# Optimization experiments

Hardware: AMD Instinct MI355X
Metric: run time of the kernel (lower is better)

Reference implementation:

```python
import jax, jax.numpy as jnp
import numpy as np

N_NODES = 50000
N_EDGES = 800000
N_GRAPHS = 512
IN_DIM = 128
HID = 64


def setup_inputs() -> dict:
    key = jax.random.key(0)
    ks = jax.random.split(key, 12)
    x = jax.random.normal(ks[0], (N_NODES, IN_DIM), dtype=jnp.float32)
    edge_index = jax.random.randint(ks[1], (2, N_EDGES), 0, N_NODES, dtype=jnp.int64)
    batch = jnp.sort(jax.random.randint(ks[2], (N_NODES,), 0, N_GRAPHS, dtype=jnp.int64))

    def lin(k, fan_in, fan_out):
        # torch Linear default init: U(-1/sqrt(fan_in), 1/sqrt(fan_in)); stored as [in, out]
        bound = 1.0 / np.sqrt(fan_in)
        return jax.random.uniform(k, (fan_in, fan_out), minval=-bound, maxval=bound, dtype=jnp.float32)

    W1_1 = lin(ks[3], IN_DIM, HID)
    W2_1 = lin(ks[4], IN_DIM, HID)
    W1_2 = lin(ks[5], HID, HID)
    W2_2 = lin(ks[6], HID, HID)
    W1_3 = lin(ks[7], HID, HID)
    W2_3 = lin(ks[8], HID, HID)
    cW1 = lin(ks[9], HID, HID)
    cb1 = jnp.zeros((HID,), dtype=jnp.float32)
    cW2 = lin(ks[10], HID, 1)
    cb2 = jnp.zeros((1,), dtype=jnp.float32)
    return {"x": x, "edge_index": edge_index, "batch": batch,
            "W1_1": W1_1, "W2_1": W2_1, "W1_2": W1_2, "W2_2": W2_2,
            "W1_3": W1_3, "W2_3": W2_3, "cW1": cW1, "cb1": cb1,
            "cW2": cW2, "cb2": cb2}


def _gnn_layer(x, src, dst, W1, W2):
    # f(v) = relu( x[v] @ W1 + sum_{u in N(v)} x[u] @ W2 )
    self_part = x @ W1                      # [N, out]
    msg = x[src] @ W2                       # gather + matmul: [E, out]
    neigh = jax.ops.segment_sum(msg, dst, num_segments=N_NODES)  # scatter-add
    return jax.nn.relu(self_part + neigh)


def reference(x, edge_index, batch, W1_1, W2_1, W1_2, W2_2, W1_3, W2_3, cW1, cb1, cW2, cb2):
    src, dst = edge_index[0], edge_index[1]  # PyG source_to_target flow
    h = _gnn_layer(x, src, dst, W1_1, W2_1)
    h = _gnn_layer(h, src, dst, W1_2, W2_2)
    h = _gnn_layer(h, src, dst, W1_3, W2_3)
    # global_mean_pool over graph segments
    sums = jax.ops.segment_sum(h, batch, num_segments=N_GRAPHS)      # [G, HID]
    counts = jax.ops.segment_sum(jnp.ones((h.shape[0],), h.dtype), batch, num_segments=N_GRAPHS)
    pooled = sums / jnp.maximum(counts, 1.0)[:, None]
    # classifier MLP
    hcls = jax.nn.relu(pooled @ cW1 + cb1)
    return hcls @ cW2 + cb2                  # [G, 1]
```

## Files before the change

### kernel.cpp

```cpp
#include <hip/hip_runtime.h>


#define CAP 64

typedef __attribute__((ext_vector_type(8))) short short8;
typedef __attribute__((ext_vector_type(4))) float floatx4;

__device__ __forceinline__ unsigned short f2bf(float f) {
    union { float f; unsigned u; } v; v.f = f;
    unsigned r = v.u + 0x7FFF + ((v.u >> 16) & 1);
    return (unsigned short)(r >> 16);
}

__device__ __forceinline__ void bf8acc(float* t, uint4 w) {
    t[0] += __uint_as_float(w.x << 16);
    t[1] += __uint_as_float(w.x & 0xffff0000u);
    t[2] += __uint_as_float(w.y << 16);
    t[3] += __uint_as_float(w.y & 0xffff0000u);
    t[4] += __uint_as_float(w.z << 16);
    t[5] += __uint_as_float(w.z & 0xffff0000u);
    t[6] += __uint_as_float(w.w << 16);
    t[7] += __uint_as_float(w.w & 0xffff0000u);
}

__device__ __forceinline__ void gather_node(
    const unsigned short* __restrict__ M, const int* __restrict__ cnt,
    const unsigned short* __restrict__ csr, int node, int cg, float* acc8)
{
    int c = cnt[node]; if (c > CAP) c = CAP;
    const uint4* bv = (const uint4*)(csr + (size_t)node * CAP);
    float a[8], b[8];
#pragma unroll
    for (int j = 0; j < 8; ++j) { a[j] = 0.f; b[j] = 0.f; }
    const int full = c >> 3;
    const int rem  = c & 7;
    for (int grp = 0; grp < full; ++grp) {
        uint4 q = bv[grp];
        unsigned idx[8];
        idx[0] = q.x & 0xffff; idx[1] = q.x >> 16;
        idx[2] = q.y & 0xffff; idx[3] = q.y >> 16;
        idx[4] = q.z & 0xffff; idx[5] = q.z >> 16;
        idx[6] = q.w & 0xffff; idx[7] = q.w >> 16;
        uint4 w[8];
#pragma unroll
        for (int j = 0; j < 8; ++j)
            w[j] = *(const uint4*)&M[(size_t)idx[j] * 64 + cg * 8];
#pragma unroll
        for (int j = 0; j < 8; ++j)
            bf8acc((j & 1) ? b : a, w[j]);
    }
    if (rem) {
        uint4 q = bv[full];
        unsigned idx[8];
        idx[0] = q.x & 0xffff; idx[1] = q.x >> 16;
        idx[2] = q.y & 0xffff; idx[3] = q.y >> 16;
        idx[4] = q.z & 0xffff; idx[5] = q.z >> 16;
        idx[6] = q.w & 0xffff; idx[7] = q.w >> 16;
#pragma unroll
        for (int j = 0; j < 7; ++j) {
            if (j < rem) {
                uint4 w = *(const uint4*)&M[(size_t)idx[j] * 64 + cg * 8];
                bf8acc((j & 1) ? b : a, w);
            }
        }
    }
#pragma unroll
    for (int j = 0; j < 8; ++j) acc8[j] = a[j] + b[j];
}


__device__ __forceinline__ void mm1_body(
    const float* __restrict__ Xraw,
    const float* __restrict__ W1, const float* __restrict__ W2,
    float* __restrict__ S, unsigned short* __restrict__ M, int N, int blk)
{
    __shared__ __align__(16) unsigned short Xs[64][72];
    __shared__ __align__(16) unsigned short Ws[128][72];
    const int tid  = threadIdx.x;
    const int lane = tid & 63;
    const int wv   = tid >> 6;
    const int lrow = lane & 15;
    const int quad = lane >> 4;
    const int row0 = blk * 64;

    floatx4 acc[8];
#pragma unroll
    for (int i = 0; i < 8; ++i) acc[i] = (floatx4){0.f, 0.f, 0.f, 0.f};

    const int xr  = tid >> 2;
    const int xk  = (tid & 3) * 16;
    const int gxr = row0 + xr;

    for (int ko = 0; ko < 128; ko += 64) {
#pragma unroll
        for (int q = 0; q < 4; ++q) {
            float4 v = make_float4(0.f, 0.f, 0.f, 0.f);
            if (gxr < N) v = *(const float4*)&Xraw[(size_t)gxr * 128 + ko + xk + q * 4];
            ushort4 p;
            p.x = f2bf(v.x); p.y = f2bf(v.y); p.z = f2bf(v.z); p.w = f2bf(v.w);
            *(ushort4*)&Xs[xr][xk + q * 4] = p;
        }
#pragma unroll
        for (int i = 0; i < 2; ++i) {
            int s  = tid + i * 256;
            int k0 = (s & 15) * 4;
            int c0 = (s >> 4) * 4;
            float wr[4][4];
#pragma unroll
            for (int r = 0; r < 4; ++r) {
                int gk = ko + k0 + r;
                float4 t4 = (c0 < 64) ? *(const float4*)&W1[(size_t)gk * 64 + c0]
                                      : *(const float4*)&W2[(size_t)gk * 64 + (c0 - 64)];
                wr[r][0] = t4.x; wr[r][1] = t4.y; wr[r][2] = t4.z; wr[r][3] = t4.w;
            }
#pragma unroll
            for (int j = 0; j < 4; ++j) {
                ushort4 col;
                col.x = f2bf(wr[0][j]); col.y = f2bf(wr[1][j]);
                col.z = f2bf(wr[2][j]); col.w = f2bf(wr[3][j]);
                *(ushort4*)&Ws[c0 + j][k0] = col;
            }
        }
        __syncthreads();

#pragma unroll
        for (int kc = 0; kc < 2; ++kc) {
            int kofs = kc * 32 + quad * 8;
            short8 a = *(const short8*)&Xs[wv * 16 + lrow][kofs];
#pragma unroll
            for (int ct = 0; ct < 8; ++ct) {
                short8 b = *(const short8*)&Ws[ct * 16 + lrow][kofs];
                acc[ct] = __builtin_amdgcn_mfma_f32_16x16x32_bf16(a, b, acc[ct], 0, 0, 0);
            }
        }
        __syncthreads();
    }

    const int orow = row0 + wv * 16 + quad * 4;
#pragma unroll
    for (int ct = 0; ct < 4; ++ct) {
        int col = ct * 16 + lrow;
#pragma unroll
        for (int r = 0; r < 4; ++r) {
            int gr = orow + r;
            if (gr < N) S[(size_t)gr * 64 + col] = acc[ct][r];
        }
    }
#pragma unroll
    for (int ct = 4; ct < 8; ++ct) {
        int col = ct * 16 + lrow - 64;
#pragma unroll
        for (int r = 0; r < 4; ++r) {
            int gr = orow + r;
            if (gr < N) M[(size_t)gr * 64 + col] = f2bf(acc[ct][r]);
        }
    }
}

__device__ __forceinline__ void fill_body(
    const int* __restrict__ ei, int* __restrict__ cnt,
    unsigned short* __restrict__ csr, int E, int bid, int stride)
{
    int base = bid * 256 + threadIdx.x;
    int e[8], d[8], s[8], p[8];
    bool v[8];
#pragma unroll
    for (int j = 0; j < 8; ++j) {
        e[j] = base + j * stride;
        v[j] = e[j] < E;
        if (v[j]) {
            d[j] = ei[E + e[j]];
            s[j] = ei[e[j]];
        }
    }
#pragma unroll
    for (int j = 0; j < 8; ++j)
        if (v[j]) p[j] = atomicAdd(&cnt[d[j]], 1);
#pragma unroll
    for (int j = 0; j < 8; ++j)
        if (v[j] && p[j] < CAP) csr[(size_t)d[j] * CAP + p[j]] = (unsigned short)s[j];
}

__global__ __launch_bounds__(256) void mm1_fill_kernel(
    const float* __restrict__ Xraw,
    const float* __restrict__ W1, const float* __restrict__ W2,
    float* __restrict__ S, unsigned short* __restrict__ M, int N,
    const int* __restrict__ ei, int* __restrict__ cnt,
    unsigned short* __restrict__ csr, int E, int edgeBlocks)
{
    if ((int)blockIdx.x < edgeBlocks) {
        fill_body(ei, cnt, csr, E, blockIdx.x, edgeBlocks * 256);
    } else {
        mm1_body(Xraw, W1, W2, S, M, N, (int)blockIdx.x - edgeBlocks);
    }
}

__global__ __launch_bounds__(256) void mm_gather_kernel(
    const float* __restrict__ Sprev, const unsigned short* __restrict__ Mprev,
    const int* __restrict__ cnt, const unsigned short* __restrict__ csr,
    const float* __restrict__ W1, const float* __restrict__ W2,
    float* __restrict__ Sout, unsigned short* __restrict__ Mout, int N)
{
    __shared__ __align__(16) unsigned short Xs[64][72];
    __shared__ __align__(16) unsigned short Ws[128][72];
    const int tid  = threadIdx.x;
    const int lane = tid & 63;
    const int wv   = tid >> 6;
    const int lrow = lane & 15;
    const int quad = lane >> 4;
    const int row0 = blockIdx.x * 64;
    const int eg   = lane >> 3;
    const int cg   = lane & 7;

#pragma unroll
    for (int i = 0; i < 2; ++i) {
        int s  = tid + i * 256;
        int k0 = (s & 15) * 4;
        int c0 = (s >> 4) * 4;
        float wr[4][4];
#pragma unroll
        for (int r = 0; r < 4; ++r) {
            int gk = k0 + r;
            float4 t4 = (c0 < 64) ? *(const float4*)&W1[(size_t)gk * 64 + c0]
                                  : *(const float4*)&W2[(size_t)gk * 64 + (c0 - 64)];
            wr[r][0] = t4.x; wr[r][1] = t4.y; wr[r][2] = t4.z; wr[r][3] = t4.w;
        }
#pragma unroll
        for (int j = 0; j < 4; ++j) {
            ushort4 col;
            col.x = f2bf(wr[0][j]); col.y = f2bf(wr[1][j]);
            col.z = f2bf(wr[2][j]); col.w = f2bf(wr[3][j]);
            *(ushort4*)&Ws[c0 + j][k0] = col;
        }
    }

#pragma unroll
    for (int half = 0; half < 2; ++half) {
        int xrow = half * 32 + wv * 8 + eg;
        int node = row0 + xrow;
        float r8[8];
        if (node < N) {
            float g8[8];
            gather_node(Mprev, cnt, csr, node, cg, g8);
            float4 s0 = *(const float4*)&Sprev[(size_t)node * 64 + cg * 8];
            float4 s1 = *(const float4*)&Sprev[(size_t)node * 64 + cg * 8 + 4];
            r8[0] = fmaxf(g8[0] + s0.x, 0.f);
            r8[1] = fmaxf(g8[1] + s0.y, 0.f);
            r8[2] = fmaxf(g8[2] + s0.z, 0.f);
            r8[3] = fmaxf(g8[3] + s0.w, 0.f);
            r8[4] = fmaxf(g8[4] + s1.x, 0.f);
            r8[5] = fmaxf(g8[5] + s1.y, 0.f);
            r8[6] = fmaxf(g8[6] + s1.z, 0.f);
            r8[7] = fmaxf(g8[7] + s1.w, 0.f);
        } else {
#pragma unroll
            for (int j = 0; j < 8; ++j) r8[j] = 0.f;
        }
        ushort4 p0, p1;
        p0.x = f2bf(r8[0]); p0.y = f2bf(r8[1]); p0.z = f2bf(r8[2]); p0.w = f2bf(r8[3]);
        p1.x = f2bf(r8[4]); p1.y = f2bf(r8[5]); p1.z = f2bf(r8[6]); p1.w = f2bf(r8[7]);
        *(ushort4*)&Xs[xrow][cg * 8]     = p0;
        *(ushort4*)&Xs[xrow][cg * 8 + 4] = p1;
    }
    __syncthreads();

    floatx4 acc[8];
#pragma unroll
    for (int i = 0; i < 8; ++i) acc[i] = (floatx4){0.f, 0.f, 0.f, 0.f};
#pragma unroll
    for (int kc = 0; kc < 2; ++kc) {
        int kofs = kc * 32 + quad * 8;
        short8 a = *(const short8*)&Xs[wv * 16 + lrow][kofs];
#pragma unroll
        for (int ct = 0; ct < 8; ++ct) {
            short8 b = *(const short8*)&Ws[ct * 16 + lrow][kofs];
            acc[ct] = __builtin_amdgcn_mfma_f32_16x16x32_bf16(a, b, acc[ct], 0, 0, 0);
        }
    }

    const int orow = row0 + wv * 16 + quad * 4;
#pragma unroll
    for (int ct = 0; ct < 4; ++ct) {
        int col = ct * 16 + lrow;
#pragma unroll
        for (int r = 0; r < 4; ++r) {
            int gr = orow + r;
            if (gr < N) Sout[(size_t)gr * 64 + col] = acc[ct][r];
        }
    }
#pragma unroll
    for (int ct = 4; ct < 8; ++ct) {
        int col = ct * 16 + lrow - 64;
#pragma unroll
        for (int r = 0; r < 4; ++r) {
            int gr = orow + r;
            if (gr < N) Mout[(size_t)gr * 64 + col] = f2bf(acc[ct][r]);
        }
    }
}

__global__ __launch_bounds__(256) void pool_gather_cls_kernel(
    const float* __restrict__ S, const unsigned short* __restrict__ M,
    const int* __restrict__ cnt, const unsigned short* __restrict__ csr,
    const int* __restrict__ batch,
    const float* __restrict__ cW1, const float* __restrict__ cb1,
    const float* __restrict__ cW2, const float* __restrict__ cb2,
    float* __restrict__ out, int N)
{
    int g  = blockIdx.x;
    int t  = threadIdx.x;
    int wv = t >> 6;
    int lane = t & 63;
    int eg = lane >> 3;
    int cg = lane & 7;

    int lo = 0, hi = N;
    while (lo < hi) { int mid = (lo + hi) >> 1; if (batch[mid] < g) lo = mid + 1; else hi = mid; }
    int start = lo;
    hi = N;
    while (lo < hi) { int mid = (lo + hi) >> 1; if (batch[mid] < g + 1) lo = mid + 1; else hi = mid; }
    int end = lo;

    float p8[8];
#pragma unroll
    for (int j = 0; j < 8; ++j) p8[j] = 0.f;

    for (int r = start + wv * 8 + eg; r < end; r += 32) {
        float g8[8];
        gather_node(M, cnt, csr, r, cg, g8);
        float4 s0 = *(const float4*)&S[(size_t)r * 64 + cg * 8];
        float4 s1 = *(const float4*)&S[(size_t)r * 64 + cg * 8 + 4];
        p8[0] += fmaxf(g8[0] + s0.x, 0.f);
        p8[1] += fmaxf(g8[1] + s0.y, 0.f);
        p8[2] += fmaxf(g8[2] + s0.z, 0.f);
        p8[3] += fmaxf(g8[3] + s0.w, 0.f);
        p8[4] += fmaxf(g8[4] + s1.x, 0.f);
        p8[5] += fmaxf(g8[5] + s1.y, 0.f);
        p8[6] += fmaxf(g8[6] + s1.z, 0.f);
        p8[7] += fmaxf(g8[7] + s1.w, 0.f);
    }

    __shared__ float part[32][64];
    __shared__ float pooled[64];
    int slot = wv * 8 + eg;
#pragma unroll
    for (int j = 0; j < 8; ++j) part[slot][cg * 8 + j] = p8[j];
    __syncthreads();

    if (t < 64) {
        float s = 0.f;
#pragma unroll 8
        for (int k = 0; k < 32; ++k) s += part[k][t];
        float c_ = (float)((end - start) > 0 ? (end - start) : 1);
        pooled[t] = s / c_;
    }
    __syncthreads();
    if (t < 64) {
        float a = cb1[t];
#pragma unroll 8
        for (int k = 0; k < 64; ++k) a += pooled[k] * cW1[k * 64 + t];
        a = fmaxf(a, 0.f);
        float o = a * cW2[t];
#pragma unroll
        for (int off_ = 32; off_ > 0; off_ >>= 1) o += __shfl_down(o, off_);
        if (t == 0) out[g] = o + cb2[0];
    }
}

extern "C" void kernel_launch(void* const* d_in, const int* in_sizes, int n_in,
                              void* d_out, int out_size, void* d_ws, size_t ws_size,
                              hipStream_t stream)
{
    const float* x     = (const float*)d_in[0];
    const int*   ei    = (const int*)d_in[1];
    const int*   batch = (const int*)d_in[2];
    const float* W1_1  = (const float*)d_in[3];
    const float* W2_1  = (const float*)d_in[4];
    const float* W1_2  = (const float*)d_in[5];
    const float* W2_2  = (const float*)d_in[6];
    const float* W1_3  = (const float*)d_in[7];
    const float* W2_3  = (const float*)d_in[8];
    const float* cW1   = (const float*)d_in[9];
    const float* cb1   = (const float*)d_in[10];
    const float* cW2   = (const float*)d_in[11];
    const float* cb2   = (const float*)d_in[12];
    float* out = (float*)d_out;

    const int N = in_sizes[0] / 128;
    const int E = in_sizes[1] / 2;
    const int G = out_size;

    float*          SA  = (float*)d_ws;
    float*          SB  = SA + (size_t)N * 64;
    unsigned short* MA  = (unsigned short*)(SB + (size_t)N * 64);
    unsigned short* MB  = MA + (size_t)N * 64;
    int*            cnt = (int*)(MB + (size_t)N * 64);
    unsigned short* csr = (unsigned short*)(cnt + N);

    const int mmGrid     = (N + 63) / 64;
    const int edgeBlocks = (E + 2047) / 2048;

    hipMemsetAsync(cnt, 0, (size_t)N * sizeof(int), stream);

    mm1_fill_kernel<<<edgeBlocks + mmGrid, 256, 0, stream>>>(
        x, W1_1, W2_1, SA, MA, N, ei, cnt, csr, E, edgeBlocks);
    mm_gather_kernel<<<mmGrid, 256, 0, stream>>>(
        SA, MA, cnt, csr, W1_2, W2_2, SB, MB, N);
    mm_gather_kernel<<<mmGrid, 256, 0, stream>>>(
        SB, MB, cnt, csr, W1_3, W2_3, SA, MA, N);
    pool_gather_cls_kernel<<<G, 256, 0, stream>>>(
        SA, MA, cnt, csr, batch, cW1, cb1, cW2, cb2, out, N);
}
```

Baseline: 221.7 us.

## Interleave two-node gathers and split pooling into node-parallel partials plus classifier

The per-node neighbor gather now handles two nodes in one loop, so each thread keeps twice as many independent loads in flight, and the Sprev loads are issued before the weight staging. The per-graph pooling kernel, which ran only G blocks each walking one graph's nodes serially, becomes a node-tiled kernel over all node blocks. Each block reduces per-graph partial sums and atomically adds them into a zeroed global buffer, and a small classifier kernel finishes the job. This trades one extra launch and float atomics (nondeterministic summation order) for much higher parallelism in the final layer.

```diff
diff --git a/kernel.cpp b/kernel.cpp
--- a/kernel.cpp
+++ b/kernel.cpp
@@ -23,49 +23,46 @@
     t[7] += __uint_as_float(w.w & 0xffff0000u);
 }
 
-__device__ __forceinline__ void gather_node(
+__device__ __forceinline__ void gather2(
     const unsigned short* __restrict__ M, const int* __restrict__ cnt,
-    const unsigned short* __restrict__ csr, int node, int cg, float* acc8)
-{
-    int c = cnt[node]; if (c > CAP) c = CAP;
-    const uint4* bv = (const uint4*)(csr + (size_t)node * CAP);
-    float a[8], b[8];
-#pragma unroll
-    for (int j = 0; j < 8; ++j) { a[j] = 0.f; b[j] = 0.f; }
-    const int full = c >> 3;
-    const int rem  = c & 7;
-    for (int grp = 0; grp < full; ++grp) {
-        uint4 q = bv[grp];
-        unsigned idx[8];
-        idx[0] = q.x & 0xffff; idx[1] = q.x >> 16;
-        idx[2] = q.y & 0xffff; idx[3] = q.y >> 16;
-        idx[4] = q.z & 0xffff; idx[5] = q.z >> 16;
-        idx[6] = q.w & 0xffff; idx[7] = q.w >> 16;
-        uint4 w[8];
+    const unsigned short* __restrict__ csr, int nodeA, int nodeB, int cg,
+    float* accA, float* accB, int N)
+{
+#pragma unroll
+    for (int j = 0; j < 8; ++j) { accA[j] = 0.f; accB[j] = 0.f; }
+    int cA = 0, cB = 0;
+    if (nodeA < N) { cA = cnt[nodeA]; cA = cA > CAP ? CAP : cA; }
+    if (nodeB < N) { cB = cnt[nodeB]; cB = cB > CAP ? CAP : cB; }
+    const uint4* bvA = (const uint4*)(csr + (size_t)nodeA * CAP);
+    const uint4* bvB = (const uint4*)(csr + (size_t)nodeB * CAP);
+    int cMax = cA > cB ? cA : cB;
+
+    for (int base = 0; base < cMax; base += 8) {
+        uint4 qA = make_uint4(0, 0, 0, 0), qB = make_uint4(0, 0, 0, 0);
+        if (base < cA) qA = bvA[base >> 3];
+        if (base < cB) qB = bvB[base >> 3];
+        unsigned iA[8], iB[8];
+        iA[0] = qA.x & 0xffff; iA[1] = qA.x >> 16;
+        iA[2] = qA.y & 0xffff; iA[3] = qA.y >> 16;
+        iA[4] = qA.z & 0xffff; iA[5] = qA.z >> 16;
+        iA[6] = qA.w & 0xffff; iA[7] = qA.w >> 16;
+        iB[0] = qB.x & 0xffff; iB[1] = qB.x >> 16;
+        iB[2] = qB.y & 0xffff; iB[3] = qB.y >> 16;
+        iB[4] = qB.z & 0xffff; iB[5] = qB.z >> 16;
+        iB[6] = qB.w & 0xffff; iB[7] = qB.w >> 16;
+        uint4 wA[8], wB[8];
 #pragma unroll
         for (int j = 0; j < 8; ++j)
-            w[j] = *(const uint4*)&M[(size_t)idx[j] * 64 + cg * 8];
+            if (base + j < cA) wA[j] = *(const uint4*)&M[(size_t)iA[j] * 64 + cg * 8];
 #pragma unroll
         for (int j = 0; j < 8; ++j)
-            bf8acc((j & 1) ? b : a, w[j]);
-    }
-    if (rem) {
-        uint4 q = bv[full];
-        unsigned idx[8];
-        idx[0] = q.x & 0xffff; idx[1] = q.x >> 16;
-        idx[2] = q.y & 0xffff; idx[3] = q.y >> 16;
-        idx[4] = q.z & 0xffff; idx[5] = q.z >> 16;
-        idx[6] = q.w & 0xffff; idx[7] = q.w >> 16;
-#pragma unroll
-        for (int j = 0; j < 7; ++j) {
-            if (j < rem) {
-                uint4 w = *(const uint4*)&M[(size_t)idx[j] * 64 + cg * 8];
-                bf8acc((j & 1) ? b : a, w);
-            }
-        }
-    }
-#pragma unroll
-    for (int j = 0; j < 8; ++j) acc8[j] = a[j] + b[j];
+            if (base + j < cB) wB[j] = *(const uint4*)&M[(size_t)iB[j] * 64 + cg * 8];
+#pragma unroll
+        for (int j = 0; j < 8; ++j) {
+            if (base + j < cA) bf8acc(accA, wA[j]);
+            if (base + j < cB) bf8acc(accB, wB[j]);
+        }
+    }
 }
 
 
@@ -212,6 +209,19 @@
     const int eg   = lane >> 3;
     const int cg   = lane & 7;
 
+    const int nodeA = row0 + wv * 8 + eg;
+    const int nodeB = nodeA + 32;
+
+    float4 sA0 = make_float4(0.f,0.f,0.f,0.f), sA1 = sA0, sB0 = sA0, sB1 = sA0;
+    if (nodeA < N) {
+        sA0 = *(const float4*)&Sprev[(size_t)nodeA * 64 + cg * 8];
+        sA1 = *(const float4*)&Sprev[(size_t)nodeA * 64 + cg * 8 + 4];
+    }
+    if (nodeB < N) {
+        sB0 = *(const float4*)&Sprev[(size_t)nodeB * 64 + cg * 8];
+        sB1 = *(const float4*)&Sprev[(size_t)nodeB * 64 + cg * 8 + 4];
+    }
+
 #pragma unroll
     for (int i = 0; i < 2; ++i) {
         int s  = tid + i * 256;
@@ -234,34 +244,28 @@
         }
     }
 
-#pragma unroll
-    for (int half = 0; half < 2; ++half) {
-        int xrow = half * 32 + wv * 8 + eg;
-        int node = row0 + xrow;
-        float r8[8];
-        if (node < N) {
-            float g8[8];
-            gather_node(Mprev, cnt, csr, node, cg, g8);
-            float4 s0 = *(const float4*)&Sprev[(size_t)node * 64 + cg * 8];
-            float4 s1 = *(const float4*)&Sprev[(size_t)node * 64 + cg * 8 + 4];
-            r8[0] = fmaxf(g8[0] + s0.x, 0.f);
-            r8[1] = fmaxf(g8[1] + s0.y, 0.f);
-            r8[2] = fmaxf(g8[2] + s0.z, 0.f);
-            r8[3] = fmaxf(g8[3] + s0.w, 0.f);
-            r8[4] = fmaxf(g8[4] + s1.x, 0.f);
-            r8[5] = fmaxf(g8[5] + s1.y, 0.f);
-            r8[6] = fmaxf(g8[6] + s1.z, 0.f);
-            r8[7] = fmaxf(g8[7] + s1.w, 0.f);
-        } else {
-#pragma unroll
-            for (int j = 0; j < 8; ++j) r8[j] = 0.f;
-        }
-        ushort4 p0, p1;
-        p0.x = f2bf(r8[0]); p0.y = f2bf(r8[1]); p0.z = f2bf(r8[2]); p0.w = f2bf(r8[3]);
-        p1.x = f2bf(r8[4]); p1.y = f2bf(r8[5]); p1.z = f2bf(r8[6]); p1.w = f2bf(r8[7]);
-        *(ushort4*)&Xs[xrow][cg * 8]     = p0;
-        *(ushort4*)&Xs[xrow][cg * 8 + 4] = p1;
-    }
+    float gA[8], gB[8];
+    gather2(Mprev, cnt, csr, nodeA, nodeB, cg, gA, gB, N);
+
+    float rA[8], rB[8];
+    rA[0] = fmaxf(gA[0] + sA0.x, 0.f); rA[1] = fmaxf(gA[1] + sA0.y, 0.f);
+    rA[2] = fmaxf(gA[2] + sA0.z, 0.f); rA[3] = fmaxf(gA[3] + sA0.w, 0.f);
+    rA[4] = fmaxf(gA[4] + sA1.x, 0.f); rA[5] = fmaxf(gA[5] + sA1.y, 0.f);
+    rA[6] = fmaxf(gA[6] + sA1.z, 0.f); rA[7] = fmaxf(gA[7] + sA1.w, 0.f);
+    rB[0] = fmaxf(gB[0] + sB0.x, 0.f); rB[1] = fmaxf(gB[1] + sB0.y, 0.f);
+    rB[2] = fmaxf(gB[2] + sB0.z, 0.f); rB[3] = fmaxf(gB[3] + sB0.w, 0.f);
+    rB[4] = fmaxf(gB[4] + sB1.x, 0.f); rB[5] = fmaxf(gB[5] + sB1.y, 0.f);
+    rB[6] = fmaxf(gB[6] + sB1.z, 0.f); rB[7] = fmaxf(gB[7] + sB1.w, 0.f);
+
+    ushort4 p0, p1;
+    p0.x = f2bf(rA[0]); p0.y = f2bf(rA[1]); p0.z = f2bf(rA[2]); p0.w = f2bf(rA[3]);
+    p1.x = f2bf(rA[4]); p1.y = f2bf(rA[5]); p1.z = f2bf(rA[6]); p1.w = f2bf(rA[7]);
+    *(ushort4*)&Xs[wv * 8 + eg][cg * 8]     = p0;
+    *(ushort4*)&Xs[wv * 8 + eg][cg * 8 + 4] = p1;
+    p0.x = f2bf(rB[0]); p0.y = f2bf(rB[1]); p0.z = f2bf(rB[2]); p0.w = f2bf(rB[3]);
+    p1.x = f2bf(rB[4]); p1.y = f2bf(rB[5]); p1.z = f2bf(rB[6]); p1.w = f2bf(rB[7]);
+    *(ushort4*)&Xs[wv * 8 + eg + 32][cg * 8]     = p0;
+    *(ushort4*)&Xs[wv * 8 + eg + 32][cg * 8 + 4] = p1;
     __syncthreads();
 
     floatx4 acc[8];
@@ -299,20 +303,74 @@
     }
 }
 
-__global__ __launch_bounds__(256) void pool_gather_cls_kernel(
+__global__ __launch_bounds__(256) void pool_partial_kernel(
     const float* __restrict__ S, const unsigned short* __restrict__ M,
     const int* __restrict__ cnt, const unsigned short* __restrict__ csr,
-    const int* __restrict__ batch,
+    const int* __restrict__ batch, float* __restrict__ gpool, int N)
+{
+    __shared__ __align__(16) float hbuf[64][68];
+    const int tid  = threadIdx.x;
+    const int lane = tid & 63;
+    const int wv   = tid >> 6;
+    const int eg   = lane >> 3;
+    const int cg   = lane & 7;
+    const int row0 = blockIdx.x * 64;
+
+    const int nodeA = row0 + wv * 8 + eg;
+    const int nodeB = nodeA + 32;
+
+    float4 sA0 = make_float4(0.f,0.f,0.f,0.f), sA1 = sA0, sB0 = sA0, sB1 = sA0;
+    if (nodeA < N) {
+        sA0 = *(const float4*)&S[(size_t)nodeA * 64 + cg * 8];
+        sA1 = *(const float4*)&S[(size_t)nodeA * 64 + cg * 8 + 4];
+    }
+    if (nodeB < N) {
+        sB0 = *(const float4*)&S[(size_t)nodeB * 64 + cg * 8];
+        sB1 = *(const float4*)&S[(size_t)nodeB * 64 + cg * 8 + 4];
+    }
+    float gA[8], gB[8];
+    gather2(M, cnt, csr, nodeA, nodeB, cg, gA, gB, N);
+
+    *(float4*)&hbuf[wv * 8 + eg][cg * 8] = make_float4(
+        fmaxf(gA[0] + sA0.x, 0.f), fmaxf(gA[1] + sA0.y, 0.f),
+        fmaxf(gA[2] + sA0.z, 0.f), fmaxf(gA[3] + sA0.w, 0.f));
+    *(float4*)&hbuf[wv * 8 + eg][cg * 8 + 4] = make_float4(
+        fmaxf(gA[4] + sA1.x, 0.f), fmaxf(gA[5] + sA1.y, 0.f),
+        fmaxf(gA[6] + sA1.z, 0.f), fmaxf(gA[7] + sA1.w, 0.f));
+    *(float4*)&hbuf[wv * 8 + eg + 32][cg * 8] = make_float4(
+        fmaxf(gB[0] + sB0.x, 0.f), fmaxf(gB[1] + sB0.y, 0.f),
+        fmaxf(gB[2] + sB0.z, 0.f), fmaxf(gB[3] + sB0.w, 0.f));
+    *(float4*)&hbuf[wv * 8 + eg + 32][cg * 8 + 4] = make_float4(
+        fmaxf(gB[4] + sB1.x, 0.f), fmaxf(gB[5] + sB1.y, 0.f),
+        fmaxf(gB[6] + sB1.z, 0.f), fmaxf(gB[7] + sB1.w, 0.f));
+    __syncthreads();
+
+    if (tid < 64 && row0 < N) {
+        int hiLim = row0 + 64 < N ? row0 + 64 : N;
+        int gfirst = batch[row0];
+        int glast  = batch[hiLim - 1];
+        for (int g = gfirst; g <= glast; ++g) {
+            int lo = row0, hi = hiLim;
+            while (lo < hi) { int mid = (lo + hi) >> 1; if (batch[mid] < g) lo = mid + 1; else hi = mid; }
+            int s0 = lo;
+            lo = row0; hi = hiLim;
+            while (lo < hi) { int mid = (lo + hi) >> 1; if (batch[mid] < g + 1) lo = mid + 1; else hi = mid; }
+            int s1 = lo;
+            float s = 0.f;
+            for (int r = s0; r < s1; ++r) s += hbuf[r - row0][tid];
+            if (s1 > s0) unsafeAtomicAdd(&gpool[g * 64 + tid], s);
+        }
+    }
+}
+
+__global__ __launch_bounds__(64) void cls_kernel(
+    const float* __restrict__ gpool, const int* __restrict__ batch,
     const float* __restrict__ cW1, const float* __restrict__ cb1,
     const float* __restrict__ cW2, const float* __restrict__ cb2,
     float* __restrict__ out, int N)
 {
-    int g  = blockIdx.x;
-    int t  = threadIdx.x;
-    int wv = t >> 6;
-    int lane = t & 63;
-    int eg = lane >> 3;
-    int cg = lane & 7;
+    int g = blockIdx.x;
+    int t = threadIdx.x;
 
     int lo = 0, hi = N;
     while (lo < hi) { int mid = (lo + hi) >> 1; if (batch[mid] < g) lo = mid + 1; else hi = mid; }
@@ -321,50 +379,19 @@
     while (lo < hi) { int mid = (lo + hi) >> 1; if (batch[mid] < g + 1) lo = mid + 1; else hi = mid; }
     int end = lo;
 
-    float p8[8];
-#pragma unroll
-    for (int j = 0; j < 8; ++j) p8[j] = 0.f;
-
-    for (int r = start + wv * 8 + eg; r < end; r += 32) {
-        float g8[8];
-        gather_node(M, cnt, csr, r, cg, g8);
-        float4 s0 = *(const float4*)&S[(size_t)r * 64 + cg * 8];
-        float4 s1 = *(const float4*)&S[(size_t)r * 64 + cg * 8 + 4];
-        p8[0] += fmaxf(g8[0] + s0.x, 0.f);
-        p8[1] += fmaxf(g8[1] + s0.y, 0.f);
-        p8[2] += fmaxf(g8[2] + s0.z, 0.f);
-        p8[3] += fmaxf(g8[3] + s0.w, 0.f);
-        p8[4] += fmaxf(g8[4] + s1.x, 0.f);
-        p8[5] += fmaxf(g8[5] + s1.y, 0.f);
-        p8[6] += fmaxf(g8[6] + s1.z, 0.f);
-        p8[7] += fmaxf(g8[7] + s1.w, 0.f);
-    }
-
-    __shared__ float part[32][64];
     __shared__ float pooled[64];
-    int slot = wv * 8 + eg;
-#pragma unroll
-    for (int j = 0; j < 8; ++j) part[slot][cg * 8 + j] = p8[j];
+    float c_ = (float)((end - start) > 0 ? (end - start) : 1);
+    pooled[t] = gpool[g * 64 + t] / c_;
     __syncthreads();
 
-    if (t < 64) {
-        float s = 0.f;
+    float a = cb1[t];
 #pragma unroll 8
-        for (int k = 0; k < 32; ++k) s += part[k][t];
-        float c_ = (float)((end - start) > 0 ? (end - start) : 1);
-        pooled[t] = s / c_;
-    }
-    __syncthreads();
-    if (t < 64) {
-        float a = cb1[t];
-#pragma unroll 8
-        for (int k = 0; k < 64; ++k) a += pooled[k] * cW1[k * 64 + t];
-        a = fmaxf(a, 0.f);
-        float o = a * cW2[t];
-#pragma unroll
-        for (int off_ = 32; off_ > 0; off_ >>= 1) o += __shfl_down(o, off_);
-        if (t == 0) out[g] = o + cb2[0];
-    }
+    for (int k = 0; k < 64; ++k) a += pooled[k] * cW1[k * 64 + t];
+    a = fmaxf(a, 0.f);
+    float o = a * cW2[t];
+#pragma unroll
+    for (int off_ = 32; off_ > 0; off_ >>= 1) o += __shfl_down(o, off_);
+    if (t == 0) out[g] = o + cb2[0];
 }
 
 extern "C" void kernel_launch(void* const* d_in, const int* in_sizes, int n_in,
@@ -390,17 +417,18 @@
     const int E = in_sizes[1] / 2;
     const int G = out_size;
 
-    float*          SA  = (float*)d_ws;
-    float*          SB  = SA + (size_t)N * 64;
-    unsigned short* MA  = (unsigned short*)(SB + (size_t)N * 64);
-    unsigned short* MB  = MA + (size_t)N * 64;
-    int*            cnt = (int*)(MB + (size_t)N * 64);
-    unsigned short* csr = (unsigned short*)(cnt + N);
+    float*          SA    = (float*)d_ws;
+    float*          SB    = SA + (size_t)N * 64;
+    unsigned short* MA    = (unsigned short*)(SB + (size_t)N * 64);
+    unsigned short* MB    = MA + (size_t)N * 64;
+    int*            cnt   = (int*)(MB + (size_t)N * 64);
+    float*          gpool = (float*)(cnt + N);
+    unsigned short* csr   = (unsigned short*)(gpool + (size_t)G * 64);
 
     const int mmGrid     = (N + 63) / 64;
     const int edgeBlocks = (E + 2047) / 2048;
 
-    hipMemsetAsync(cnt, 0, (size_t)N * sizeof(int), stream);
+    hipMemsetAsync(cnt, 0, (size_t)N * sizeof(int) + (size_t)G * 64 * sizeof(float), stream);
 
     mm1_fill_kernel<<<edgeBlocks + mmGrid, 256, 0, stream>>>(
         x, W1_1, W2_1, SA, MA, N, ei, cnt, csr, E, edgeBlocks);
@@ -408,6 +436,7 @@
         SA, MA, cnt, csr, W1_2, W2_2, SB, MB, N);
     mm_gather_kernel<<<mmGrid, 256, 0, stream>>>(
         SB, MB, cnt, csr, W1_3, W2_3, SA, MA, N);
-    pool_gather_cls_kernel<<<G, 256, 0, stream>>>(
-        SA, MA, cnt, csr, batch, cW1, cb1, cW2, cb2, out, N);
-}
+    pool_partial_kernel<<<mmGrid, 256, 0, stream>>>(
+        SA, MA, cnt, csr, batch, gpool, N);
+    cls_kernel<<<G, 64, 0, stream>>>(gpool, batch, cW1, cb1, cW2, cb2, out, N);
+}
```

Result: slower. 269.2 us (+21.4%).

## Build per-node edge buckets via linked lists instead of atomic-add scatter

Applied to the files above, without the earlier changes.

Replaces the atomicAdd-count plus direct scatter into fixed-capacity buckets with a two-phase build. First, atomicExch pushes each edge onto a per-destination linked list (head/next arrays). Then a separate kernel walks each node's list to fill the bucket and count. This trades scattered 2-byte stores during the fill for pointer-chasing serial walks per node, and adds an extra kernel launch and more workspace. Edge order within buckets becomes nondeterministic in a different way.

```diff
diff --git a/kernel.cpp b/kernel.cpp
--- a/kernel.cpp
+++ b/kernel.cpp
@@ -157,42 +157,59 @@
     }
 }
 
-__device__ __forceinline__ void fill_body(
-    const int* __restrict__ ei, int* __restrict__ cnt,
-    unsigned short* __restrict__ csr, int E, int bid, int stride)
+__device__ __forceinline__ void fillA_body(
+    const int* __restrict__ ei, int* __restrict__ head,
+    int* __restrict__ nxt, int E, int bid, int stride)
 {
     int base = bid * 256 + threadIdx.x;
-    int e[8], d[8], s[8], p[8];
+    int e[8], d[8], o[8];
     bool v[8];
 #pragma unroll
     for (int j = 0; j < 8; ++j) {
         e[j] = base + j * stride;
         v[j] = e[j] < E;
-        if (v[j]) {
-            d[j] = ei[E + e[j]];
-            s[j] = ei[e[j]];
-        }
+        if (v[j]) d[j] = ei[E + e[j]];
     }
 #pragma unroll
     for (int j = 0; j < 8; ++j)
-        if (v[j]) p[j] = atomicAdd(&cnt[d[j]], 1);
+        if (v[j]) o[j] = atomicExch(&head[d[j]], e[j]);
 #pragma unroll
     for (int j = 0; j < 8; ++j)
-        if (v[j] && p[j] < CAP) csr[(size_t)d[j] * CAP + p[j]] = (unsigned short)s[j];
+        if (v[j]) nxt[e[j]] = o[j];
 }
 
 __global__ __launch_bounds__(256) void mm1_fill_kernel(
     const float* __restrict__ Xraw,
     const float* __restrict__ W1, const float* __restrict__ W2,
     float* __restrict__ S, unsigned short* __restrict__ M, int N,
-    const int* __restrict__ ei, int* __restrict__ cnt,
-    unsigned short* __restrict__ csr, int E, int edgeBlocks)
+    const int* __restrict__ ei, int* __restrict__ head,
+    int* __restrict__ nxt, int E, int edgeBlocks)
 {
     if ((int)blockIdx.x < edgeBlocks) {
-        fill_body(ei, cnt, csr, E, blockIdx.x, edgeBlocks * 256);
+        fillA_body(ei, head, nxt, E, blockIdx.x, edgeBlocks * 256);
     } else {
         mm1_body(Xraw, W1, W2, S, M, N, (int)blockIdx.x - edgeBlocks);
     }
+}
+
+__global__ __launch_bounds__(256) void listB_kernel(
+    const int* __restrict__ ei, const int* __restrict__ head,
+    const int* __restrict__ nxt, unsigned short* __restrict__ csr,
+    int* __restrict__ cnt, int N, int E)
+{
+    int v = blockIdx.x * 256 + threadIdx.x;
+    if (v >= N) return;
+    unsigned short* bkt = csr + (size_t)v * CAP;
+    int p = head[v];
+    int c = 0;
+    while (p >= 0 && c < CAP) {
+        int nx = nxt[p];
+        int src = ei[p];
+        bkt[c] = (unsigned short)src;
+        ++c;
+        p = nx;
+    }
+    cnt[v] = c;
 }
 
 __global__ __launch_bounds__(256) void mm_gather_kernel(
@@ -390,20 +407,24 @@
     const int E = in_sizes[1] / 2;
     const int G = out_size;
 
-    float*          SA  = (float*)d_ws;
-    float*          SB  = SA + (size_t)N * 64;
-    unsigned short* MA  = (unsigned short*)(SB + (size_t)N * 64);
-    unsigned short* MB  = MA + (size_t)N * 64;
-    int*            cnt = (int*)(MB + (size_t)N * 64);
-    unsigned short* csr = (unsigned short*)(cnt + N);
+    float*          SA   = (float*)d_ws;
+    float*          SB   = SA + (size_t)N * 64;
+    unsigned short* MA   = (unsigned short*)(SB + (size_t)N * 64);
+    unsigned short* MB   = MA + (size_t)N * 64;
+    int*            head = (int*)(MB + (size_t)N * 64);
+    int*            nxt  = head + N;
+    int*            cnt  = nxt + E;
+    unsigned short* csr  = (unsigned short*)(cnt + N);
 
     const int mmGrid     = (N + 63) / 64;
     const int edgeBlocks = (E + 2047) / 2048;
-
-    hipMemsetAsync(cnt, 0, (size_t)N * sizeof(int), stream);
+    const int bGrid      = (N + 255) / 256;
+
+    hipMemsetAsync(head, 0xFF, (size_t)N * sizeof(int), stream);
 
     mm1_fill_kernel<<<edgeBlocks + mmGrid, 256, 0, stream>>>(
-        x, W1_1, W2_1, SA, MA, N, ei, cnt, csr, E, edgeBlocks);
+        x, W1_1, W2_1, SA, MA, N, ei, head, nxt, E, edgeBlocks);
+    listB_kernel<<<bGrid, 256, 0, stream>>>(ei, head, nxt, csr, cnt, N, E);
     mm_gather_kernel<<<mmGrid, 256, 0, stream>>>(
         SA, MA, cnt, csr, W1_2, W2_2, SB, MB, N);
     mm_gather_kernel<<<mmGrid, 256, 0, stream>>>(
```

New measurement: 234.6 us. 5.8% more time.

## Issue first 16 neighbor gathers unconditionally with masked FMA; widen pool kernel

Applied to the files above, without the earlier changes.

The neighbor gather now always loads the first two CSR index groups and 16 neighbor rows up front. It masks invalid entries by multiplying with zero instead of branching, so more independent loads are in flight per thread. Out-of-range nodes are clamped to node 0 so the gather runs without a branch. The pool/classifier kernel moves to 512 threads with 64 partial slots, and the workspace buffers are reordered. The cost is extra wasted loads for low-degree nodes and higher register pressure from 16 uint4 loads held at once.

```diff
diff --git a/kernel.cpp b/kernel.cpp
--- a/kernel.cpp
+++ b/kernel.cpp
@@ -12,57 +12,64 @@
     return (unsigned short)(r >> 16);
 }
 
-__device__ __forceinline__ void bf8acc(float* t, uint4 w) {
-    t[0] += __uint_as_float(w.x << 16);
-    t[1] += __uint_as_float(w.x & 0xffff0000u);
-    t[2] += __uint_as_float(w.y << 16);
-    t[3] += __uint_as_float(w.y & 0xffff0000u);
-    t[4] += __uint_as_float(w.z << 16);
-    t[5] += __uint_as_float(w.z & 0xffff0000u);
-    t[6] += __uint_as_float(w.w << 16);
-    t[7] += __uint_as_float(w.w & 0xffff0000u);
-}
-
-__device__ __forceinline__ void gather_node(
+__device__ __forceinline__ void bf8fma(float* t, uint4 w, float s) {
+    t[0] = fmaf(__uint_as_float(w.x << 16),          s, t[0]);
+    t[1] = fmaf(__uint_as_float(w.x & 0xffff0000u),  s, t[1]);
+    t[2] = fmaf(__uint_as_float(w.y << 16),          s, t[2]);
+    t[3] = fmaf(__uint_as_float(w.y & 0xffff0000u),  s, t[3]);
+    t[4] = fmaf(__uint_as_float(w.z << 16),          s, t[4]);
+    t[5] = fmaf(__uint_as_float(w.z & 0xffff0000u),  s, t[5]);
+    t[6] = fmaf(__uint_as_float(w.w << 16),          s, t[6]);
+    t[7] = fmaf(__uint_as_float(w.w & 0xffff0000u),  s, t[7]);
+}
+
+__device__ __forceinline__ void gather_deep(
     const unsigned short* __restrict__ M, const int* __restrict__ cnt,
-    const unsigned short* __restrict__ csr, int node, int cg, float* acc8)
-{
-    int c = cnt[node]; if (c > CAP) c = CAP;
-    const uint4* bv = (const uint4*)(csr + (size_t)node * CAP);
+    const unsigned short* __restrict__ csr, int node, int cg, float* acc8, int N)
+{
+    const int nodeC = node < N ? node : 0;
+    int c = node < N ? cnt[nodeC] : 0;
+    if (c > CAP) c = CAP;
+    const uint4* bv = (const uint4*)(csr + (size_t)nodeC * CAP);
+
+    uint4 q0 = bv[0];
+    uint4 q1 = bv[1];
+    unsigned idx[16];
+    idx[0]  = q0.x & 0xffff; idx[1]  = q0.x >> 16;
+    idx[2]  = q0.y & 0xffff; idx[3]  = q0.y >> 16;
+    idx[4]  = q0.z & 0xffff; idx[5]  = q0.z >> 16;
+    idx[6]  = q0.w & 0xffff; idx[7]  = q0.w >> 16;
+    idx[8]  = q1.x & 0xffff; idx[9]  = q1.x >> 16;
+    idx[10] = q1.y & 0xffff; idx[11] = q1.y >> 16;
+    idx[12] = q1.z & 0xffff; idx[13] = q1.z >> 16;
+    idx[14] = q1.w & 0xffff; idx[15] = q1.w >> 16;
+
+    uint4 w[16];
+#pragma unroll
+    for (int j = 0; j < 16; ++j)
+        w[j] = *(const uint4*)&M[(size_t)idx[j] * 64 + cg * 8];
+
     float a[8], b[8];
 #pragma unroll
     for (int j = 0; j < 8; ++j) { a[j] = 0.f; b[j] = 0.f; }
-    const int full = c >> 3;
-    const int rem  = c & 7;
-    for (int grp = 0; grp < full; ++grp) {
-        uint4 q = bv[grp];
-        unsigned idx[8];
-        idx[0] = q.x & 0xffff; idx[1] = q.x >> 16;
-        idx[2] = q.y & 0xffff; idx[3] = q.y >> 16;
-        idx[4] = q.z & 0xffff; idx[5] = q.z >> 16;
-        idx[6] = q.w & 0xffff; idx[7] = q.w >> 16;
-        uint4 w[8];
+#pragma unroll
+    for (int j = 0; j < 16; ++j)
+        bf8fma((j & 1) ? b : a, w[j], (j < c) ? 1.f : 0.f);
+
+    for (int base = 16; base < c; base += 8) {
+        uint4 q = bv[base >> 3];
+        unsigned id2[8];
+        id2[0] = q.x & 0xffff; id2[1] = q.x >> 16;
+        id2[2] = q.y & 0xffff; id2[3] = q.y >> 16;
+        id2[4] = q.z & 0xffff; id2[5] = q.z >> 16;
+        id2[6] = q.w & 0xffff; id2[7] = q.w >> 16;
+        uint4 w2[8];
 #pragma unroll
         for (int j = 0; j < 8; ++j)
-            w[j] = *(const uint4*)&M[(size_t)idx[j] * 64 + cg * 8];
+            w2[j] = *(const uint4*)&M[(size_t)id2[j] * 64 + cg * 8];
 #pragma unroll
         for (int j = 0; j < 8; ++j)
-            bf8acc((j & 1) ? b : a, w[j]);
-    }
-    if (rem) {
-        uint4 q = bv[full];
-        unsigned idx[8];
-        idx[0] = q.x & 0xffff; idx[1] = q.x >> 16;
-        idx[2] = q.y & 0xffff; idx[3] = q.y >> 16;
-        idx[4] = q.z & 0xffff; idx[5] = q.z >> 16;
-        idx[6] = q.w & 0xffff; idx[7] = q.w >> 16;
-#pragma unroll
-        for (int j = 0; j < 7; ++j) {
-            if (j < rem) {
-                uint4 w = *(const uint4*)&M[(size_t)idx[j] * 64 + cg * 8];
-                bf8acc((j & 1) ? b : a, w);
-            }
-        }
+            bf8fma((j & 1) ? b : a, w2[j], (base + j < c) ? 1.f : 0.f);
     }
 #pragma unroll
     for (int j = 0; j < 8; ++j) acc8[j] = a[j] + b[j];
@@ -238,10 +245,10 @@
     for (int half = 0; half < 2; ++half) {
         int xrow = half * 32 + wv * 8 + eg;
         int node = row0 + xrow;
+        float g8[8];
+        gather_deep(Mprev, cnt, csr, node, cg, g8, N);
         float r8[8];
         if (node < N) {
-            float g8[8];
-            gather_node(Mprev, cnt, csr, node, cg, g8);
             float4 s0 = *(const float4*)&Sprev[(size_t)node * 64 + cg * 8];
             float4 s1 = *(const float4*)&Sprev[(size_t)node * 64 + cg * 8 + 4];
             r8[0] = fmaxf(g8[0] + s0.x, 0.f);
@@ -299,7 +306,7 @@
     }
 }
 
-__global__ __launch_bounds__(256) void pool_gather_cls_kernel(
+__global__ __launch_bounds__(512) void pool_gather_cls_kernel(
     const float* __restrict__ S, const unsigned short* __restrict__ M,
     const int* __restrict__ cnt, const unsigned short* __restrict__ csr,
     const int* __restrict__ batch,
@@ -313,6 +320,7 @@
     int lane = t & 63;
     int eg = lane >> 3;
     int cg = lane & 7;
+    int slot = wv * 8 + eg;
 
     int lo = 0, hi = N;
     while (lo < hi) { int mid = (lo + hi) >> 1; if (batch[mid] < g) lo = mid + 1; else hi = mid; }
@@ -325,9 +333,9 @@
 #pragma unroll
     for (int j = 0; j < 8; ++j) p8[j] = 0.f;
 
-    for (int r = start + wv * 8 + eg; r < end; r += 32) {
+    for (int r = start + slot; r < end; r += 64) {
         float g8[8];
-        gather_node(M, cnt, csr, r, cg, g8);
+        gather_deep(M, cnt, csr, r, cg, g8, N);
         float4 s0 = *(const float4*)&S[(size_t)r * 64 + cg * 8];
         float4 s1 = *(const float4*)&S[(size_t)r * 64 + cg * 8 + 4];
         p8[0] += fmaxf(g8[0] + s0.x, 0.f);
@@ -340,9 +348,8 @@
         p8[7] += fmaxf(g8[7] + s1.w, 0.f);
     }
 
-    __shared__ float part[32][64];
+    __shared__ float part[64][64];
     __shared__ float pooled[64];
-    int slot = wv * 8 + eg;
 #pragma unroll
     for (int j = 0; j < 8; ++j) part[slot][cg * 8 + j] = p8[j];
     __syncthreads();
@@ -350,7 +357,7 @@
     if (t < 64) {
         float s = 0.f;
 #pragma unroll 8
-        for (int k = 0; k < 32; ++k) s += part[k][t];
+        for (int k = 0; k < 64; ++k) s += part[k][t];
         float c_ = (float)((end - start) > 0 ? (end - start) : 1);
         pooled[t] = s / c_;
     }
@@ -391,10 +398,10 @@
     const int G = out_size;
 
     float*          SA  = (float*)d_ws;
-    float*          SB  = SA + (size_t)N * 64;
-    unsigned short* MA  = (unsigned short*)(SB + (size_t)N * 64);
+    unsigned short* MA  = (unsigned short*)(SA + (size_t)N * 64);
     unsigned short* MB  = MA + (size_t)N * 64;
-    int*            cnt = (int*)(MB + (size_t)N * 64);
+    float*          SB  = (float*)(MB + (size_t)N * 64);
+    int*            cnt = (int*)(SB + (size_t)N * 64);
     unsigned short* csr = (unsigned short*)(cnt + N);
 
     const int mmGrid     = (N + 63) / 64;
@@ -408,6 +415,6 @@
         SA, MA, cnt, csr, W1_2, W2_2, SB, MB, N);
     mm_gather_kernel<<<mmGrid, 256, 0, stream>>>(
         SB, MB, cnt, csr, W1_3, W2_3, SA, MA, N);
-    pool_gather_cls_kernel<<<G, 256, 0, stream>>>(
+    pool_gather_cls_kernel<<<G, 512, 0, stream>>>(
         SA, MA, cnt, csr, batch, cW1, cb1, cW2, cb2, out, N);
 }
```

After: 216.5 us. 2.3% less time.
